# Performance work log

Measured on AMD Instinct MI355X. Metric: run time of the kernel, lower is better.

Reference implementation:

```python
import math
import jax, jax.numpy as jnp
import numpy as np

N = 50000
C = 128      # in_channels == out_channels
H = 8        # nhead
D = C // H   # head_dim = 16
E = 800000


def _layernorm(x, g, b, eps=1e-5):
    mu = jnp.mean(x, axis=-1, keepdims=True)
    var = jnp.var(x, axis=-1, keepdims=True)
    return (x - mu) * jax.lax.rsqrt(var + eps) * g + b


def setup_inputs() -> dict:
    key = jax.random.key(0)
    ks = jax.random.split(key, 12)
    s = 1.0 / math.sqrt(C)          # ~xavier scale
    s4 = 1.0 / math.sqrt(4 * C)
    return {
        "x": jax.random.normal(ks[0], (N, C), dtype=jnp.float32),
        "edge_index": jax.random.randint(ks[1], (2, E), 0, N, dtype=jnp.int64),
        "Wq": jax.random.normal(ks[2], (C, C), dtype=jnp.float32) * s,
        "Wk": jax.random.normal(ks[3], (C, C), dtype=jnp.float32) * s,
        "Wv": jax.random.normal(ks[4], (C, C), dtype=jnp.float32) * s,
        "Wo": jax.random.normal(ks[5], (C, C), dtype=jnp.float32) * s,
        "bo": jnp.zeros((C,), dtype=jnp.float32),
        "Wf1": jax.random.normal(ks[6], (C, 4 * C), dtype=jnp.float32) * s,
        "bf1": jnp.zeros((4 * C,), dtype=jnp.float32),
        "Wf2": jax.random.normal(ks[7], (4 * C, C), dtype=jnp.float32) * s4,
        "bf2": jnp.zeros((C,), dtype=jnp.float32),
        "g1": jnp.ones((C,), dtype=jnp.float32),
        "b1": jnp.zeros((C,), dtype=jnp.float32),
        "g2": jnp.ones((C,), dtype=jnp.float32),
        "b2": jnp.zeros((C,), dtype=jnp.float32),
    }


def reference(x, edge_index, Wq, Wk, Wv, Wo, bo, Wf1, bf1, Wf2, bf2, g1, b1, g2, b2):
    n = x.shape[0]
    loops = jnp.arange(n, dtype=edge_index.dtype)
    row = jnp.concatenate([edge_index[0], loops])  # source nodes
    col = jnp.concatenate([edge_index[1], loops])  # destination nodes

    q = (x @ Wq).reshape(n, H, D)
    k = (x @ Wk).reshape(n, H, D)
    v = (x @ Wv).reshape(n, H, D)

    # edge-level attention scores [E+N, H]
    scores = jnp.einsum('ehd,ehd->eh', q[row], k[col]) / math.sqrt(D)
    smax = jax.ops.segment_max(scores, col, num_segments=n)  # every node has a self-loop
    exp = jnp.exp(scores - smax[col])
    ssum = jax.ops.segment_sum(exp, col, num_segments=n)
    alpha = exp / (ssum[col] + 1e-8)

    out = jax.ops.segment_sum(v[row] * alpha[..., None], col, num_segments=n)
    attn = out.reshape(n, C) @ Wo + bo

    residual = x  # input_proj is Identity (in_channels == out_channels)
    x1 = _layernorm(residual + attn, g1, b1)
    ffn = jax.nn.gelu(x1 @ Wf1 + bf1, approximate=False) @ Wf2 + bf2
    return _layernorm(x1 + ffn, g2, b2)
```

## Files before the change

### kernel.cpp

```cpp
#include <hip/hip_runtime.h>
#include <cmath>


typedef short bf16x8 __attribute__((ext_vector_type(8)));
typedef float f32x4 __attribute__((ext_vector_type(4)));
typedef unsigned int uint_as1 __attribute__((address_space(1)));
typedef unsigned int uint_as3 __attribute__((address_space(3)));

__device__ inline unsigned short f2bf(float f) {
    unsigned int u = __float_as_uint(f);
    u += 0x7fffu + ((u >> 16) & 1u);
    return (unsigned short)(u >> 16);
}
__device__ inline float bflo(unsigned int w) { return __uint_as_float(w << 16); }
__device__ inline float bfhi(unsigned int w) { return __uint_as_float(w & 0xffff0000u); }

__device__ inline void gload16(const unsigned short* g, unsigned short* l) {
    __builtin_amdgcn_global_load_lds((const uint_as1*)g, (uint_as3*)l, 16, 0, 0);
}

__device__ inline float gelu_f(float x) {
    float ax = fabsf(x) * 0.70710678118f;
    float t = __builtin_amdgcn_rcpf(fmaf(0.3275911f, ax, 1.0f));
    float p = fmaf(1.061405429f, t, -1.453152027f);
    p = fmaf(p, t, 1.421413741f);
    p = fmaf(p, t, -0.284496736f);
    p = fmaf(p, t, 0.254829592f);
    p = p * t;
    float e = __expf(-ax * ax);
    float pe = p * e;
    float w = (x >= 0.f) ? (2.0f - pe) : pe;
    return 0.5f * x * w;
}


__device__ __forceinline__ void stage_panel(unsigned short* Bs,
                                            const unsigned short* base,
                                            int strideK) {
    int tid = threadIdx.x;
    int srow = tid >> 4, cc = tid & 15;
    int gc = (cc & ~7) | ((cc & 7) ^ (srow & 7));
    const unsigned short* src = base + (size_t)srow * strideK + gc * 8;
    unsigned short* dst = Bs + srow * 128 + cc * 8;
#pragma unroll
    for (int j = 0; j < 8; ++j)
        gload16(src + (size_t)j * 16 * strideK, dst + j * 16 * 128);
}

__device__ __forceinline__ void loadA16(bf16x8 (&af)[4],
                                        const unsigned short* A, int M, int K,
                                        int base, int ko, int l16, int quad) {
    int row = base + l16;
    if (row > M - 1) row = M - 1;
    const unsigned short* ar = A + (size_t)row * K + ko + quad * 8;
#pragma unroll
    for (int j = 0; j < 4; ++j) af[j] = *(const bf16x8*)(ar + j * 32);
}

__device__ __forceinline__ void loadA_k(bf16x8 (&af)[4][4],
                                        const unsigned short* A, int M, int K,
                                        int m0, int ko, int wr, int l16, int quad) {
#pragma unroll
    for (int ti = 0; ti < 4; ++ti) {
        int row = m0 + wr * 64 + ti * 16 + l16;
        if (row > M - 1) row = M - 1;
        const unsigned short* ar = A + (size_t)row * K + ko + quad * 8;
#pragma unroll
        for (int j = 0; j < 4; ++j) af[ti][j] = *(const bf16x8*)(ar + j * 32);
    }
}

__device__ __forceinline__ void mm16(f32x4 (&acc)[4][4], const bf16x8 (&af)[4][4],
                                     const unsigned short* Bs,
                                     int wc, int quad, int l16) {
#pragma unroll
    for (int ks = 0; ks < 4; ++ks) {
        bf16x8 bfr[4];
#pragma unroll
        for (int tj = 0; tj < 4; ++tj) {
            int nr = wc * 64 + tj * 16 + l16;
            int cidx = ks * 4 + quad;
            int slot = (cidx & ~7) | ((cidx & 7) ^ (nr & 7));
            bfr[tj] = *(const bf16x8*)&Bs[nr * 128 + slot * 8];
        }
#pragma unroll
        for (int ti = 0; ti < 4; ++ti)
#pragma unroll
            for (int tj = 0; tj < 4; ++tj)
                acc[ti][tj] = __builtin_amdgcn_mfma_f32_16x16x32_bf16(
                    af[ti][ks], bfr[tj], acc[ti][tj], 0, 0, 0);
    }
}


__global__ __launch_bounds__(256) void k_init(
    const float* __restrict__ x, unsigned short* __restrict__ xb,
    const float* __restrict__ Wq, const float* __restrict__ Wk,
    const float* __restrict__ Wv, const float* __restrict__ Wo,
    const float* __restrict__ Wf1, const float* __restrict__ Wf2,
    unsigned short* __restrict__ Wqkvt, unsigned short* __restrict__ Wot,
    unsigned short* __restrict__ Wf1t, unsigned short* __restrict__ Wf2t,
    int* __restrict__ cursor, int4* __restrict__ csrz,
    int N, int nCsr4, int nCast) {
    int bid = blockIdx.x;
    int t = threadIdx.x;

    int NBc = (N + 255) >> 8;
    if (bid < NBc) {
        int i = bid * 256 + t;
        if (i < N) cursor[i] = 0;
        return;
    }
    bid -= NBc;
    int NBz = (nCsr4 + 255) >> 8;
    if (bid < NBz) {
        int i = bid * 256 + t;
        if (i < nCsr4) csrz[i] = make_int4(0, 0, 0, 0);
        return;
    }
    bid -= NBz;
    if (bid < nCast) {
        int i = bid * 256 + t;
        if (i < N * 32) {
            float4 v = ((const float4*)x)[i];
            ushort4 o;
            o.x = f2bf(v.x); o.y = f2bf(v.y); o.z = f2bf(v.z); o.w = f2bf(v.w);
            ((ushort4*)xb)[i] = o;
        }
        return;
    }
    bid -= nCast;
    int z, idx;
    if (bid < 256) { z = bid >> 6; idx = (bid & 63) * 256 + t; }
    else           { z = 4 + ((bid - 256) >> 8); idx = ((bid - 256) & 255) * 256 + t; }

    const float* in; unsigned short* out; int K, Co;
    switch (z) {
        case 0: in = Wq;  out = Wqkvt; K = 128; Co = 128; break;
        case 1: in = Wk;  out = Wqkvt; K = 128; Co = 128; break;
        case 2: in = Wv;  out = Wqkvt; K = 128; Co = 128; break;
        case 3: in = Wo;  out = Wot;   K = 128; Co = 128; break;
        case 4: in = Wf1; out = Wf1t;  K = 128; Co = 512; break;
        default: in = Wf2; out = Wf2t; K = 512; Co = 128; break;
    }
    if (idx >= K * Co) return;
    int k = idx / Co, c = idx % Co;
    int row;
    switch (z) {
        case 0: row = ((c >> 1) << 2) | (c & 1); break;
        case 1: row = 256 + c; break;
        case 2: row = (((c >> 1) << 2) | (c & 1)) + 2; break;
        default: row = c; break;
    }
    out[(size_t)row * K + k] = f2bf(in[idx]);
}


__global__ void k_fill(const int* __restrict__ ei, int* __restrict__ cursor,
                       unsigned short* __restrict__ csr, int E, int N,
                       int NB, int Rng) {
    int pass = blockIdx.x / NB;
    int e = (blockIdx.x - pass * NB) * 256 + threadIdx.x;
    if (e >= E + N) return;
    int lo = pass * Rng, hi = lo + Rng;
    int col = (e < E) ? ei[E + e] : (e - E);
    if (col < lo || col >= hi) return;
    int row = (e < E) ? ei[e] : col;
    int pos = atomicAdd(&cursor[col], 1);
    csr[(size_t)col * 64 + pos] = (unsigned short)row;
}


template <int EPI>
__global__ __launch_bounds__(256) void k_gemmP(
    const unsigned short* __restrict__ A, const unsigned short* __restrict__ Bt,
    const float* __restrict__ bias, const float* __restrict__ resid,
    const float* __restrict__ g, const float* __restrict__ b,
    float* __restrict__ outf, unsigned short* __restrict__ outb,
    int M, int Cout, int NZ) {
    __shared__ unsigned short Bs[128 * 128];

    int tid = threadIdx.x;
    int w = tid >> 6, lane = tid & 63;
    int quad = lane >> 4, l16 = lane & 15;
    int zi = blockIdx.x % NZ;
    int ci = blockIdx.x / NZ;
    int n0 = zi * 128;

    stage_panel(Bs, Bt + (size_t)n0 * 128, 128);

    float bi[8], gv[8], bv[8];
    if constexpr (EPI >= 1) {
#pragma unroll
        for (int tj = 0; tj < 8; ++tj) bi[tj] = bias[n0 * (EPI == 1) + tj * 16 + l16];
    }
    if constexpr (EPI == 2) {
#pragma unroll
        for (int tj = 0; tj < 8; ++tj) {
            gv[tj] = g[tj * 16 + l16];
            bv[tj] = b[tj * 16 + l16];
        }
    }

    int base0 = ci * 128 + w * 16;
    int base1 = base0 + 64;
    bf16x8 afA[4], afB[4];
    loadA16(afA, A, M, 128, base0, 0, l16, quad);
    loadA16(afB, A, M, 128, base1, 0, l16, quad);
    __syncthreads();

    auto tile = [&](const bf16x8 (&af)[4], int base) {
        f32x4 acc[8];
#pragma unroll
        for (int tj = 0; tj < 8; ++tj) acc[tj] = {0.f, 0.f, 0.f, 0.f};
#pragma unroll
        for (int ks = 0; ks < 4; ++ks) {
            int cidx = ks * 4 + quad;
#pragma unroll
            for (int tj = 0; tj < 8; ++tj) {
                int nr = tj * 16 + l16;
                int slot = (cidx & ~7) | ((cidx & 7) ^ (nr & 7));
                bf16x8 bfr = *(const bf16x8*)&Bs[nr * 128 + slot * 8];
                acc[tj] = __builtin_amdgcn_mfma_f32_16x16x32_bf16(
                    af[ks], bfr, acc[tj], 0, 0, 0);
            }
        }
        if constexpr (EPI == 0) {
#pragma unroll
            for (int tj = 0; tj < 8; ++tj) {
                int col = n0 + tj * 16 + l16;
#pragma unroll
                for (int r = 0; r < 4; ++r) {
                    int row = base + quad * 4 + r;
                    if (row < M) outb[(size_t)row * Cout + col] = f2bf(acc[tj][r]);
                }
            }
        } else if constexpr (EPI == 1) {
#pragma unroll
            for (int tj = 0; tj < 8; ++tj) {
                int col = n0 + tj * 16 + l16;
#pragma unroll
                for (int r = 0; r < 4; ++r) {
                    int row = base + quad * 4 + r;
                    if (row < M)
                        outb[(size_t)row * Cout + col] = f2bf(gelu_f(acc[tj][r] + bi[tj]));
                }
            }
        } else {
#pragma unroll
            for (int tj = 0; tj < 8; ++tj) {
                int col = tj * 16 + l16;
#pragma unroll
                for (int r = 0; r < 4; ++r) {
                    int row = base + quad * 4 + r;
                    float rv = (row < M) ? resid[(size_t)row * 128 + col] : 0.f;
                    acc[tj][r] += bi[tj] + rv;
                }
            }
#pragma unroll
            for (int r = 0; r < 4; ++r) {
                float s = 0.f, q = 0.f;
#pragma unroll
                for (int tj = 0; tj < 8; ++tj) {
                    s += acc[tj][r];
                    q += acc[tj][r] * acc[tj][r];
                }
                s += __shfl_xor(s, 1); q += __shfl_xor(q, 1);
                s += __shfl_xor(s, 2); q += __shfl_xor(q, 2);
                s += __shfl_xor(s, 4); q += __shfl_xor(q, 4);
                s += __shfl_xor(s, 8); q += __shfl_xor(q, 8);
                float mean = s * 0.0078125f;
                float var = q * 0.0078125f - mean * mean;
                float rs = rsqrtf(var + 1e-5f);
                int row = base + quad * 4 + r;
                bool ok = row < M;
#pragma unroll
                for (int tj = 0; tj < 8; ++tj) {
                    int col = tj * 16 + l16;
                    float y = (acc[tj][r] - mean) * rs * gv[tj] + bv[tj];
                    if (ok) {
                        outf[(size_t)row * 128 + col] = y;
                        outb[(size_t)row * 128 + col] = f2bf(y);
                    }
                }
            }
        }
    };

    tile(afA, base0);
    tile(afB, base1);
}


template <int KT>
__global__ __launch_bounds__(256) void k_gemmK(
    const unsigned short* __restrict__ A, const unsigned short* __restrict__ Bt,
    const float* __restrict__ bias, const float* __restrict__ resid,
    const float* __restrict__ g, const float* __restrict__ b,
    float* __restrict__ outf, int M) {
    constexpr int K = KT * 128;
    __shared__ unsigned short smem[128 * 128];
    __shared__ float pS[2][128], pQ[2][128];

    int tid = threadIdx.x;
    int wid = tid >> 6, lane = tid & 63;
    int quad = lane >> 4, l16 = lane & 15;
    int wr = wid >> 1, wc = wid & 1;
    int m0 = blockIdx.x * 128;

    f32x4 acc[4][4];
#pragma unroll
    for (int i = 0; i < 4; ++i)
#pragma unroll
        for (int j = 0; j < 4; ++j) acc[i][j] = {0.f, 0.f, 0.f, 0.f};

#pragma unroll
    for (int kt = 0; kt < KT; ++kt) {
        bf16x8 af[4][4];
        loadA_k(af, A, M, K, m0, kt * 128, wr, l16, quad);
        stage_panel(smem, Bt + kt * 128, K);
        __syncthreads();
        mm16(acc, af, smem, wc, quad, l16);
        __syncthreads();
    }

    float bi[4], gv[4], bv[4];
#pragma unroll
    for (int tj = 0; tj < 4; ++tj) {
        int col = wc * 64 + tj * 16 + l16;
        bi[tj] = bias[col]; gv[tj] = g[col]; bv[tj] = b[col];
    }
#pragma unroll
    for (int ti = 0; ti < 4; ++ti)
#pragma unroll
        for (int tj = 0; tj < 4; ++tj) {
            int col = wc * 64 + tj * 16 + l16;
#pragma unroll
            for (int r = 0; r < 4; ++r) {
                int row = m0 + wr * 64 + ti * 16 + quad * 4 + r;
                float rv = (row < M) ? resid[(size_t)row * 128 + col] : 0.f;
                acc[ti][tj][r] += bi[tj] + rv;
            }
        }
#pragma unroll
    for (int ti = 0; ti < 4; ++ti)
#pragma unroll
        for (int r = 0; r < 4; ++r) {
            float s = acc[ti][0][r] + acc[ti][1][r] + acc[ti][2][r] + acc[ti][3][r];
            float q = acc[ti][0][r] * acc[ti][0][r] + acc[ti][1][r] * acc[ti][1][r]
                    + acc[ti][2][r] * acc[ti][2][r] + acc[ti][3][r] * acc[ti][3][r];
            s += __shfl_xor(s, 1); q += __shfl_xor(q, 1);
            s += __shfl_xor(s, 2); q += __shfl_xor(q, 2);
            s += __shfl_xor(s, 4); q += __shfl_xor(q, 4);
            s += __shfl_xor(s, 8); q += __shfl_xor(q, 8);
            if (l16 == 0) {
                int lr = wr * 64 + ti * 16 + quad * 4 + r;
                pS[wc][lr] = s; pQ[wc][lr] = q;
            }
        }
    __syncthreads();
    if (tid < 128) {
        float s = pS[0][tid] + pS[1][tid];
        float q = pQ[0][tid] + pQ[1][tid];
        float mean = s * 0.0078125f;
        float var = q * 0.0078125f - mean * mean;
        pS[0][tid] = mean;
        pQ[0][tid] = rsqrtf(var + 1e-5f);
    }
    __syncthreads();
#pragma unroll
    for (int ti = 0; ti < 4; ++ti)
#pragma unroll
        for (int r = 0; r < 4; ++r) {
            int lr = wr * 64 + ti * 16 + quad * 4 + r;
            int row = m0 + lr;
            if (row >= M) continue;
            float mean = pS[0][lr], rs = pQ[0][lr];
#pragma unroll
            for (int tj = 0; tj < 4; ++tj) {
                int col = wc * 64 + tj * 16 + l16;
                outf[(size_t)row * 128 + col] =
                    (acc[ti][tj][r] - mean) * rs * gv[tj] + bv[tj];
            }
        }
}


__global__ __launch_bounds__(256) void k_attn(
    const unsigned int* __restrict__ qkv, const int* __restrict__ counts,
    const unsigned short* __restrict__ csr, unsigned int* __restrict__ ob,
    int N) {
    int j = blockIdx.x * 4 + (threadIdx.x >> 6);
    if (j >= N) return;
    int l = threadIdx.x & 63;
    int lk = l & 31;
    int half = l >> 5;
    const uint4* qv4 = (const uint4*)qkv;

    uint2 kw = *(const uint2*)(qkv + (size_t)j * 192 + 128 + lk * 2);
    const float S = 0.36067376022224085f;
    float k0 = bflo(kw.x) * S, k1 = bfhi(kw.x) * S;
    float k2 = bflo(kw.y) * S, k3 = bfhi(kw.y) * S;

    int cnt = counts[j];
    int nb = (cnt + 3) >> 2;
    const unsigned short* cp = csr + (size_t)j * 64;

    int ra0 = cp[half],     rb0 = cp[2 + half];
    int ra1 = cp[4 + half], rb1 = cp[6 + half];
    uint4 gA = qv4[(unsigned)ra0 * 48u + lk];
    uint4 gB = qv4[(unsigned)rb0 * 48u + lk];

    float lsum = 0.f, a0 = 0.f, a1 = 0.f, a2 = 0.f, a3 = 0.f;
    for (int bi = 0; bi < nb; ++bi) {
        int ra2 = cp[(bi + 2) * 4 + half];
        int rb2 = cp[(bi + 2) * 4 + 2 + half];
        uint4 nA = qv4[(unsigned)ra1 * 48u + lk];
        uint4 nB = qv4[(unsigned)rb1 * 48u + lk];

        int rem = cnt - bi * 4;
        {
            float s = fmaf(bflo(gA.x), k0,
                      fmaf(bfhi(gA.x), k1,
                      fmaf(bflo(gA.z), k2, bfhi(gA.z) * k3)));
            s += __shfl_xor(s, 1);
            s += __shfl_xor(s, 2);
            float e = exp2f(s);
            e = (half < rem) ? e : 0.f;
            lsum += e;
            a0 = fmaf(e, bflo(gA.y), a0); a1 = fmaf(e, bfhi(gA.y), a1);
            a2 = fmaf(e, bflo(gA.w), a2); a3 = fmaf(e, bfhi(gA.w), a3);
        }
        {
            float s = fmaf(bflo(gB.x), k0,
                      fmaf(bfhi(gB.x), k1,
                      fmaf(bflo(gB.z), k2, bfhi(gB.z) * k3)));
            s += __shfl_xor(s, 1);
            s += __shfl_xor(s, 2);
            float e = exp2f(s);
            e = (2 + half < rem) ? e : 0.f;
            lsum += e;
            a0 = fmaf(e, bflo(gB.y), a0); a1 = fmaf(e, bfhi(gB.y), a1);
            a2 = fmaf(e, bflo(gB.w), a2); a3 = fmaf(e, bfhi(gB.w), a3);
        }
        gA = nA; gB = nB; ra1 = ra2; rb1 = rb2;
    }

    lsum += __shfl_xor(lsum, 32);
    a0 += __shfl_xor(a0, 32); a1 += __shfl_xor(a1, 32);
    a2 += __shfl_xor(a2, 32); a3 += __shfl_xor(a3, 32);

    if (half == 0) {
        float inv = 1.f / (lsum + 1e-8f);
        uint2 o;
        o.x = ((unsigned int)f2bf(a1 * inv) << 16) | (unsigned int)f2bf(a0 * inv);
        o.y = ((unsigned int)f2bf(a3 * inv) << 16) | (unsigned int)f2bf(a2 * inv);
        *(uint2*)(ob + (size_t)j * 64 + lk * 2) = o;
    }
}


extern "C" void kernel_launch(void* const* d_in, const int* in_sizes, int n_in,
                              void* d_out, int out_size, void* d_ws, size_t ws_size,
                              hipStream_t stream) {
    const float* x   = (const float*)d_in[0];
    const int* ei    = (const int*)d_in[1];
    const float* Wq  = (const float*)d_in[2];
    const float* Wk  = (const float*)d_in[3];
    const float* Wv  = (const float*)d_in[4];
    const float* Wo  = (const float*)d_in[5];
    const float* bo  = (const float*)d_in[6];
    const float* Wf1 = (const float*)d_in[7];
    const float* bf1 = (const float*)d_in[8];
    const float* Wf2 = (const float*)d_in[9];
    const float* bf2 = (const float*)d_in[10];
    const float* g1  = (const float*)d_in[11];
    const float* b1  = (const float*)d_in[12];
    const float* g2  = (const float*)d_in[13];
    const float* b2  = (const float*)d_in[14];

    int N = in_sizes[0] / 128;
    int E = in_sizes[1] / 2;
    int N2 = ((N + 127) / 128) * 128;
    int NE = E + N;

    char* p = (char*)d_ws;
    auto alloc = [&](size_t bytes) -> char* {
        char* r = p;
        p += (bytes + 255) & ~(size_t)255;
        return r;
    };
    unsigned short* qkv = (unsigned short*)alloc((size_t)N2 * 512 * 2);
    unsigned short* ob  = qkv + (size_t)N2 * 384;
    unsigned short* hb  = qkv;
    unsigned short* x1b = (unsigned short*)alloc((size_t)N2 * 128 * 2);
    unsigned short* xb  = x1b;
    float* x1f          = (float*)alloc((size_t)N2 * 128 * 4);
    unsigned short* Wqkvt = (unsigned short*)alloc(384 * 128 * 2);
    unsigned short* Wot   = (unsigned short*)alloc(128 * 128 * 2);
    unsigned short* Wf1t  = (unsigned short*)alloc(512 * 128 * 2);
    unsigned short* Wf2t  = (unsigned short*)alloc(128 * 512 * 2);
    int* cursor = (int*)alloc((size_t)N * 4);
    unsigned short* csr = (unsigned short*)alloc(((size_t)N * 64 + 256) * 2);

    int nCsr4 = N * 8 + 32;
    int nCast = (N * 32 + 255) / 256;
    int nInit = ((N + 255) / 256) + ((nCsr4 + 255) / 256) + nCast + 768;
    int M128 = (N + 127) / 128;
    int NB = (NE + 255) / 256;
    int Rng = (N + 7) / 8;

    k_init<<<nInit, 256, 0, stream>>>(x, xb, Wq, Wk, Wv, Wo, Wf1, Wf2,
                                      Wqkvt, Wot, Wf1t, Wf2t,
                                      cursor, (int4*)csr, N, nCsr4, nCast);
    k_fill<<<8 * NB, 256, 0, stream>>>(ei, cursor, csr, E, N, NB, Rng);

    k_gemmP<0><<<3 * M128, 256, 0, stream>>>(
        xb, Wqkvt, nullptr, nullptr, nullptr, nullptr, nullptr, qkv,
        N, 384, 3);

    k_attn<<<(N + 3) / 4, 256, 0, stream>>>((const unsigned int*)qkv, cursor,
                                            csr, (unsigned int*)ob, N);

    k_gemmP<2><<<M128, 256, 0, stream>>>(
        ob, Wot, bo, x, g1, b1, x1f, x1b, N, 128, 1);

    k_gemmP<1><<<4 * M128, 256, 0, stream>>>(
        x1b, Wf1t, bf1, nullptr, nullptr, nullptr, nullptr, hb, N, 512, 4);

    k_gemmK<4><<<M128, 256, 0, stream>>>(
        hb, Wf2t, bf2, x1f, g2, b2, (float*)d_out, N);
}
```

Measured before the change: 313.1 us.

## Fuse CSR fill and QKV projection GEMM into one interleaved launch

Merges the edge-to-CSR atomic fill kernel and the QKV projection GEMM into a single kernel. One in every 24 blocks does a 128-row GEMM tile and the rest do the CSR fill, so the compute-bound GEMM can overlap the atomic- and latency-bound scatter and one launch is removed. The GEMM blocks now read weight fragments straight from global memory (through cache) instead of staging them in swizzled shared memory. That may lower GEMM efficiency, and the fill blocks inherit the heavier register footprint of the fused kernel, which could cut their occupancy.

Measured after the change: 505.3 us. 1.61x slower.

```diff
diff --git a/kernel.cpp b/kernel.cpp
--- a/kernel.cpp
+++ b/kernel.cpp
@@ -156,18 +156,70 @@
 }
 
 
-__global__ void k_fill(const int* __restrict__ ei, int* __restrict__ cursor,
-                       unsigned short* __restrict__ csr, int E, int N,
-                       int NB, int Rng) {
-    int pass = blockIdx.x / NB;
-    int e = (blockIdx.x - pass * NB) * 256 + threadIdx.x;
-    if (e >= E + N) return;
-    int lo = pass * Rng, hi = lo + Rng;
-    int col = (e < E) ? ei[E + e] : (e - E);
-    if (col < lo || col >= hi) return;
-    int row = (e < E) ? ei[e] : col;
-    int pos = atomicAdd(&cursor[col], 1);
-    csr[(size_t)col * 64 + pos] = (unsigned short)row;
+__global__ __launch_bounds__(256) void k_fq(
+    const int* __restrict__ ei, int* __restrict__ cursor,
+    unsigned short* __restrict__ csr, int E, int N, int NB, int Rng,
+    const unsigned short* __restrict__ xb,
+    const unsigned short* __restrict__ Wqkvt,
+    unsigned short* __restrict__ qkv, int Mt) {
+    int bid = blockIdx.x;
+
+    if (bid % 24) {
+        int fi = bid - bid / 24 - 1;
+        int pass = fi / NB;
+        if (pass >= 8) return;
+        int e = (fi - pass * NB) * 256 + threadIdx.x;
+        if (e >= E + N) return;
+        int lo = pass * Rng, hi = lo + Rng;
+        int col = (e < E) ? ei[E + e] : (e - E);
+        if (col < lo || col >= hi) return;
+        int row = (e < E) ? ei[e] : col;
+        int pos = atomicAdd(&cursor[col], 1);
+        csr[(size_t)col * 64 + pos] = (unsigned short)row;
+        return;
+    }
+
+    int qb = bid / 24;
+    int zi = qb % 3, ci = qb / 3;
+    int n0 = zi * 128;
+    int tid = threadIdx.x;
+    int w = tid >> 6, lane = tid & 63;
+    int quad = lane >> 4, l16 = lane & 15;
+    const unsigned short* Bp = Wqkvt + (size_t)n0 * 128;
+
+    int base0 = ci * 128 + w * 16;
+    int base1 = base0 + 64;
+    bf16x8 afA[4], afB[4];
+    loadA16(afA, xb, N, 128, base0, 0, l16, quad);
+    loadA16(afB, xb, N, 128, base1, 0, l16, quad);
+
+    auto tileg = [&](const bf16x8 (&af)[4], int base) {
+        f32x4 acc[8];
+#pragma unroll
+        for (int tj = 0; tj < 8; ++tj) acc[tj] = {0.f, 0.f, 0.f, 0.f};
+#pragma unroll
+        for (int ks = 0; ks < 4; ++ks) {
+            int co = (ks * 4 + quad) * 8;
+#pragma unroll
+            for (int tj = 0; tj < 8; ++tj) {
+                bf16x8 bfr = *(const bf16x8*)&Bp[(size_t)(tj * 16 + l16) * 128 + co];
+                acc[tj] = __builtin_amdgcn_mfma_f32_16x16x32_bf16(
+                    af[ks], bfr, acc[tj], 0, 0, 0);
+            }
+        }
+#pragma unroll
+        for (int tj = 0; tj < 8; ++tj) {
+            int col = n0 + tj * 16 + l16;
+#pragma unroll
+            for (int r = 0; r < 4; ++r) {
+                int row = base + quad * 4 + r;
+                if (row < N) qkv[(size_t)row * 384 + col] = f2bf(acc[tj][r]);
+            }
+        }
+    };
+
+    tileg(afA, base0);
+    tileg(afB, base1);
 }
 
 
@@ -225,17 +277,7 @@
                     af[ks], bfr, acc[tj], 0, 0, 0);
             }
         }
-        if constexpr (EPI == 0) {
-#pragma unroll
-            for (int tj = 0; tj < 8; ++tj) {
-                int col = n0 + tj * 16 + l16;
-#pragma unroll
-                for (int r = 0; r < 4; ++r) {
-                    int row = base + quad * 4 + r;
-                    if (row < M) outb[(size_t)row * Cout + col] = f2bf(acc[tj][r]);
-                }
-            }
-        } else if constexpr (EPI == 1) {
+        if constexpr (EPI == 1) {
 #pragma unroll
             for (int tj = 0; tj < 8; ++tj) {
                 int col = n0 + tj * 16 + l16;
@@ -513,11 +555,9 @@
     k_init<<<nInit, 256, 0, stream>>>(x, xb, Wq, Wk, Wv, Wo, Wf1, Wf2,
                                       Wqkvt, Wot, Wf1t, Wf2t,
                                       cursor, (int4*)csr, N, nCsr4, nCast);
-    k_fill<<<8 * NB, 256, 0, stream>>>(ei, cursor, csr, E, N, NB, Rng);
-
-    k_gemmP<0><<<3 * M128, 256, 0, stream>>>(
-        xb, Wqkvt, nullptr, nullptr, nullptr, nullptr, nullptr, qkv,
-        N, 384, 3);
+
+    k_fq<<<24 * 3 * M128, 256, 0, stream>>>(ei, cursor, csr, E, N, NB, Rng,
+                                            xb, Wqkvt, qkv, M128);
 
     k_attn<<<(N + 3) / 4, 256, 0, stream>>>((const unsigned int*)qkv, cursor,
                                             csr, (unsigned int*)ob, N);
```
